# Kernel tuning notes

Hardware: AMD Instinct MI355X
Metric: run time of the kernel (lower is better)

The kernel has to match this reference:

```python
import jax, jax.numpy as jnp
import numpy as np

B, C, H, W = 4, 128, 512, 512
NUM_LABELS = 512  # superpixels per frame; matches fill_max of label_maps


def setup_inputs() -> dict:
    key = jax.random.key(0)
    k1, k2 = jax.random.split(key)
    x = jax.random.normal(k1, (B, C, H, W), dtype=jnp.float32)
    label_maps = jax.random.randint(k2, (B, 1, H, W), 0, NUM_LABELS, dtype=jnp.int64)
    return {"x": x, "label_maps": label_maps}


def reference(x, label_maps):
    """Per-image, per-superpixel-label mean pooling (use_max=False).

    x:          [B, C, H, W] float features
    label_maps: [B, 1, H, W] int superpixel labels in [0, NUM_LABELS)
    returns:    [B, NUM_LABELS, C] mean feature per superpixel
    """
    Bv, Cv, Hv, Wv = x.shape
    P = Hv * Wv
    xf = x.reshape(Bv, Cv, P).transpose(0, 2, 1)          # [B, P, C]
    lab = label_maps[:, 0].reshape(Bv, P)                  # [B, P]

    def per_image(xi, li):
        # xi: [P, C], li: [P]
        sums = jax.ops.segment_sum(xi, li, num_segments=NUM_LABELS)      # [L, C]
        ones = jnp.ones((P,), dtype=xi.dtype)
        cnt = jax.ops.segment_sum(ones, li, num_segments=NUM_LABELS)     # [L]
        return sums / jnp.maximum(cnt, 1.0)[:, None]                      # [L, C]

    return jax.vmap(per_image)(xf, lab)
```

## Files before the change

kernel.cpp:

```cpp
#include <hip/hip_runtime.h>


constexpr int Bn = 4, Cn = 128, Hn = 512, Wn = 512;
constexpr int Pn = Hn * Wn;
constexpr int Ln = 512;
constexpr int CPB = 32;
constexpr int CG = Cn / CPB;
constexpr int SPLITS = 32;
constexpr int NPIX = Pn / SPLITS;
constexpr int CPW = 8;

__global__ void zero_kernel(float4* __restrict__ out4, int* __restrict__ counts) {
    const int i = blockIdx.x * 256 + threadIdx.x;
    out4[i] = float4{0.f, 0.f, 0.f, 0.f};
    if (i < Bn * Ln) counts[i] = 0;
}

__global__ void count_kernel(const int* __restrict__ labels, int* __restrict__ counts) {
    __shared__ int cnt[Ln];
    const int b   = blockIdx.x >> 4;
    const int blk = blockIdx.x & 15;
    for (int i = threadIdx.x; i < Ln; i += 256) cnt[i] = 0;
    __syncthreads();
    const int4* lab4 = (const int4*)(labels + b * Pn + blk * (Pn / 16));
#pragma unroll
    for (int it = 0; it < (Pn / 16) / (4 * 256); ++it) {
        int4 l = lab4[it * 256 + threadIdx.x];
        atomicAdd(&cnt[l.x], 1);
        atomicAdd(&cnt[l.y], 1);
        atomicAdd(&cnt[l.z], 1);
        atomicAdd(&cnt[l.w], 1);
    }
    __syncthreads();
    for (int i = threadIdx.x; i < Ln; i += 256)
        atomicAdd(&counts[b * Ln + i], cnt[i]);
}

__global__ void __launch_bounds__(256, 2)
sum_kernel(const float* __restrict__ x, const int* __restrict__ labels,
           float* __restrict__ out) {
    __shared__ float acc[CPB * Ln];

    const int bid = blockIdx.x;
    const int ps  = bid & (SPLITS - 1);
    const int cg  = (bid >> 5) & (CG - 1);
    const int b   = bid >> 7;

    for (int i = threadIdx.x; i < CPB * Ln; i += 256) acc[i] = 0.f;
    __syncthreads();

    const int wave = threadIdx.x >> 6;
    const int lane = threadIdx.x & 63;
    const int p0   = ps * NPIX;

    const int4* lab4 = (const int4*)(labels + b * Pn + p0);
    const float4* xp[CPW];
    float* accl[CPW];
#pragma unroll
    for (int j = 0; j < CPW; ++j) {
        const int c_local = wave * CPW + j;
        xp[j]   = (const float4*)(x + (size_t)(b * Cn + cg * CPB + c_local) * Pn + p0);
        accl[j] = acc + c_local * Ln;
    }

    for (int it = 0; it < NPIX / (64 * 4); ++it) {
        const int idx = it * 64 + lane;
        const int4 l = lab4[idx];
#pragma unroll
        for (int j = 0; j < CPW; ++j) {
            const float4 v = xp[j][idx];
            atomicAdd(&accl[j][l.x], v.x);
            atomicAdd(&accl[j][l.y], v.y);
            atomicAdd(&accl[j][l.z], v.z);
            atomicAdd(&accl[j][l.w], v.w);
        }
    }
    __syncthreads();

    for (int i = threadIdx.x; i < CPB * Ln; i += 256) {
        const int l = i >> 5;
        const int c_local = i & 31;
        atomicAdd(&out[((size_t)b * Ln + l) * Cn + cg * CPB + c_local],
                  acc[c_local * Ln + l]);
    }
}

__global__ void div_kernel(float4* __restrict__ out4, const int* __restrict__ counts) {
    const int i = blockIdx.x * 256 + threadIdx.x;
    const int bl = i >> 5;
    const float inv = 1.0f / fmaxf((float)counts[bl], 1.0f);
    float4 v = out4[i];
    v.x *= inv; v.y *= inv; v.z *= inv; v.w *= inv;
    out4[i] = v;
}

extern "C" void kernel_launch(void* const* d_in, const int* in_sizes, int n_in,
                              void* d_out, int out_size, void* d_ws, size_t ws_size,
                              hipStream_t stream) {
    const float* x      = (const float*)d_in[0];
    const int*   labels = (const int*)d_in[1];
    float* out  = (float*)d_out;
    int* counts = (int*)d_ws;

    zero_kernel <<<(Bn * Ln * Cn / 4) / 256, 256, 0, stream>>>((float4*)out, counts);
    count_kernel<<<Bn * 16,                  256, 0, stream>>>(labels, counts);
    sum_kernel  <<<Bn * CG * SPLITS,         256, 0, stream>>>(x, labels, out);
    div_kernel  <<<(Bn * Ln * Cn / 4) / 256, 256, 0, stream>>>((float4*)out, counts);
}
```

Before: 1.216 ms.

## Stage feature tiles through LDS with direct global-to-LDS loads and transposed accumulator

```diff
diff --git a/kernel.cpp b/kernel.cpp
--- a/kernel.cpp
+++ b/kernel.cpp
@@ -6,9 +6,16 @@
 constexpr int Ln = 512;
 constexpr int CPB = 32;
 constexpr int CG = Cn / CPB;
-constexpr int SPLITS = 32;
+constexpr int SPLITS = 16;
 constexpr int NPIX = Pn / SPLITS;
-constexpr int CPW = 8;
+constexpr int TP = 256;
+constexpr int NT = NPIX / TP;
+constexpr int CB = 64;
+
+#define GLD_LDS16(gsrc, ldst)                                        \
+    __builtin_amdgcn_global_load_lds(                                \
+        (const __attribute__((address_space(1))) void*)(gsrc),       \
+        (__attribute__((address_space(3))) void*)(ldst), 16, 0, 0)
 
 __global__ void zero_kernel(float4* __restrict__ out4, int* __restrict__ counts) {
     const int i = blockIdx.x * 256 + threadIdx.x;
@@ -18,13 +25,13 @@
 
 __global__ void count_kernel(const int* __restrict__ labels, int* __restrict__ counts) {
     __shared__ int cnt[Ln];
-    const int b   = blockIdx.x >> 4;
-    const int blk = blockIdx.x & 15;
+    const int b   = blockIdx.x >> 6;
+    const int blk = blockIdx.x & 63;
     for (int i = threadIdx.x; i < Ln; i += 256) cnt[i] = 0;
     __syncthreads();
-    const int4* lab4 = (const int4*)(labels + b * Pn + blk * (Pn / 16));
+    const int4* lab4 = (const int4*)(labels + (size_t)b * Pn + blk * (Pn / CB));
 #pragma unroll
-    for (int it = 0; it < (Pn / 16) / (4 * 256); ++it) {
+    for (int it = 0; it < (Pn / CB) / (4 * 256); ++it) {
         int4 l = lab4[it * 256 + threadIdx.x];
         atomicAdd(&cnt[l.x], 1);
         atomicAdd(&cnt[l.y], 1);
@@ -36,52 +43,67 @@
         atomicAdd(&counts[b * Ln + i], cnt[i]);
 }
 
-__global__ void __launch_bounds__(256, 2)
+__global__ void __launch_bounds__(256, 1)
 sum_kernel(const float* __restrict__ x, const int* __restrict__ labels,
            float* __restrict__ out) {
-    __shared__ float acc[CPB * Ln];
+    __shared__ float acc[Ln * CPB];
+    __shared__ float tile[CPB * TP];
+    __shared__ int   labt[TP];
 
     const int bid = blockIdx.x;
     const int ps  = bid & (SPLITS - 1);
-    const int cg  = (bid >> 5) & (CG - 1);
-    const int b   = bid >> 7;
+    const int cg  = (bid >> 4) & (CG - 1);
+    const int b   = bid >> 6;
+    const int p0  = ps * NPIX;
 
-    for (int i = threadIdx.x; i < CPB * Ln; i += 256) acc[i] = 0.f;
-    __syncthreads();
+    float4* acc4 = (float4*)acc;
+    for (int i = threadIdx.x; i < Ln * CPB / 4; i += 256)
+        acc4[i] = float4{0.f, 0.f, 0.f, 0.f};
 
     const int wave = threadIdx.x >> 6;
     const int lane = threadIdx.x & 63;
-    const int p0   = ps * NPIX;
 
-    const int4* lab4 = (const int4*)(labels + b * Pn + p0);
-    const float4* xp[CPW];
-    float* accl[CPW];
+    const float* src[8];
 #pragma unroll
-    for (int j = 0; j < CPW; ++j) {
-        const int c_local = wave * CPW + j;
-        xp[j]   = (const float4*)(x + (size_t)(b * Cn + cg * CPB + c_local) * Pn + p0);
-        accl[j] = acc + c_local * Ln;
+    for (int j = 0; j < 8; ++j) {
+        const int r = wave * 8 + j;
+        src[j] = x + (size_t)(b * Cn + cg * CPB + r) * Pn + p0 + ((lane ^ j) << 2);
+    }
+    const int* labsrc = labels + (size_t)b * Pn + p0 + (lane << 2);
+
+    const int c  = lane & 31;
+    const int s  = lane >> 5;
+    const int c7 = c & 7;
+    float* accc  = acc + c;
+    const float* trow = tile + c * TP;
+
+    __syncthreads();
+
+    for (int t = 0; t < NT; ++t) {
+#pragma unroll
+        for (int j = 0; j < 8; ++j)
+            GLD_LDS16(src[j] + t * TP, tile + (wave * 8 + j) * TP);
+        if (wave == 0)
+            GLD_LDS16(labsrc + t * TP, labt);
+        __syncthreads();
+
+#pragma unroll
+        for (int k = 0; k < 8; ++k) {
+            const int p4 = wave * 16 + k * 2 + s;
+            const float4 v = *(const float4*)(trow + ((p4 ^ c7) << 2));
+            const int4 l4  = *(const int4*)(labt + (p4 << 2));
+            atomicAdd(accc + (l4.x << 5), v.x);
+            atomicAdd(accc + (l4.y << 5), v.y);
+            atomicAdd(accc + (l4.z << 5), v.z);
+            atomicAdd(accc + (l4.w << 5), v.w);
+        }
+        __syncthreads();
     }
 
-    for (int it = 0; it < NPIX / (64 * 4); ++it) {
-        const int idx = it * 64 + lane;
-        const int4 l = lab4[idx];
-#pragma unroll
-        for (int j = 0; j < CPW; ++j) {
-            const float4 v = xp[j][idx];
-            atomicAdd(&accl[j][l.x], v.x);
-            atomicAdd(&accl[j][l.y], v.y);
-            atomicAdd(&accl[j][l.z], v.z);
-            atomicAdd(&accl[j][l.w], v.w);
-        }
-    }
-    __syncthreads();
-
     for (int i = threadIdx.x; i < CPB * Ln; i += 256) {
-        const int l = i >> 5;
-        const int c_local = i & 31;
-        atomicAdd(&out[((size_t)b * Ln + l) * Cn + cg * CPB + c_local],
-                  acc[c_local * Ln + l]);
+        const int l = i >> 5, cl = i & 31;
+        atomicAdd(&out[((size_t)b * Ln + l) * Cn + cg * CPB + cl],
+                  acc[(l << 5) + cl]);
     }
 }
 
@@ -103,7 +125,7 @@
     int* counts = (int*)d_ws;
 
     zero_kernel <<<(Bn * Ln * Cn / 4) / 256, 256, 0, stream>>>((float4*)out, counts);
-    count_kernel<<<Bn * 16,                  256, 0, stream>>>(labels, counts);
+    count_kernel<<<Bn * CB,                  256, 0, stream>>>(labels, counts);
     sum_kernel  <<<Bn * CG * SPLITS,         256, 0, stream>>>(x, labels, out);
     div_kernel  <<<(Bn * Ln * Cn / 4) / 256, 256, 0, stream>>>((float4*)out, counts);
 }
```

After: 1.292 ms. 6.3% more time.
